# Kernel optimization log

Hardware: AMD Instinct MI355X
Metric: run time of the kernel (lower is better)

## Reference

```python
import jax, jax.numpy as jnp
import numpy as np

B, C, H, W = 4, 512, 64, 64
D = 512  # model_dim


def setup_inputs() -> dict:
    key = jax.random.key(0)
    ks = jax.random.split(key, 9)
    s = 0.02
    return {
        "q": jax.random.normal(ks[0], (B, C, H, W), dtype=jnp.float32),
        "Wq": jax.random.normal(ks[1], (D, C), dtype=jnp.float32) * s,
        "bq": jax.random.normal(ks[2], (D,), dtype=jnp.float32) * s,
        "Wk": jax.random.normal(ks[3], (D, C), dtype=jnp.float32) * s,
        "bk": jax.random.normal(ks[4], (D,), dtype=jnp.float32) * s,
        "Wv": jax.random.normal(ks[5], (D, C), dtype=jnp.float32) * s,
        "bv": jax.random.normal(ks[6], (D,), dtype=jnp.float32) * s,
        "Wo": jax.random.normal(ks[7], (C, D), dtype=jnp.float32) * s,
        "bo": jax.random.normal(ks[8], (C,), dtype=jnp.float32) * s,
    }


def reference(q, Wq, bq, Wk, bk, Wv, bv, Wo, bo):
    b, c, h, w = q.shape
    # 1x1 conv == per-pixel linear over channels; tokens s = h*w
    x = q.reshape(b, c, h * w)                      # (b, c, s)
    Q = jnp.einsum('bcs,dc->bsd', x, Wq) + bq       # (b, s, D)
    K = jnp.einsum('bcs,dc->bsd', x, Wk) + bk
    V = jnp.einsum('bcs,dc->bsd', x, Wv) + bv
    # ScaleAttend: scale = q.shape[-1]^-0.5 = model_dim^-0.5 (heads not split)
    scale = jnp.asarray(Q.shape[-1], Q.dtype) ** -0.5
    sim = jnp.einsum('bsd,btd->bst', Q, K) * scale  # (b, s, s)
    attn = jax.nn.softmax(sim, axis=-1)
    o = jnp.einsum('bst,btd->bsd', attn, V)         # (b, s, D)
    # to_out 1x1 conv: D -> C
    y = jnp.einsum('bsd,cd->bsc', o, Wo) + bo       # (b, s, C)
    return y.transpose(0, 2, 1).reshape(b, c, h, w)
```

## Files before the change

kernel.cpp:

```cpp
#include <hip/hip_runtime.h>
#include <hip/hip_bf16.h>

typedef __hip_bfloat16 bf16;
typedef __attribute__((ext_vector_type(8))) short short8;
typedef __attribute__((ext_vector_type(4))) float floatx4;
typedef __attribute__((ext_vector_type(4))) short shortx4;

static constexpr int BATCH = 4;
static constexpr int CH    = 512;
static constexpr int SEQ   = 4096;
static constexpr int DM    = 512;

__device__ __forceinline__ void gload16(const void* g, void* l) {
  __builtin_amdgcn_global_load_lds(
      (const __attribute__((address_space(1))) unsigned int*)g,
      (__attribute__((address_space(3))) unsigned int*)l,
      16, 0, 0);
}

__global__ __launch_bounds__(256) void cvt_weights(
    const float* __restrict__ w0, const float* __restrict__ w1,
    const float* __restrict__ w2, const float* __restrict__ w3,
    bf16* __restrict__ out) {
  const float* src = (blockIdx.y == 0) ? w0 : (blockIdx.y == 1) ? w1
                   : (blockIdx.y == 2) ? w2 : w3;
  int idx = blockIdx.x * 256 + threadIdx.x;
  out[(long)blockIdx.y * (DM * CH) + idx] = __float2bfloat16(src[idx]);
}

__global__ __launch_bounds__(256) void transpose_cvt(
    const float* __restrict__ x, bf16* __restrict__ xT) {
  __shared__ float tile[64][65];
  const int s0 = blockIdx.x * 64, c0 = blockIdx.y * 64;
  const float* xb = x + (long)blockIdx.z * CH * SEQ;
  bf16* xTb = xT + (long)blockIdx.z * SEQ * CH;
  const int t = threadIdx.x;
  const int sl = t & 63, cq = t >> 6;
  #pragma unroll
  for (int i = 0; i < 16; ++i) {
    int cl = cq * 16 + i;
    tile[cl][sl] = xb[(long)(c0 + cl) * SEQ + s0 + sl];
  }
  __syncthreads();
  const int cl2 = t & 63, sq = t >> 6;
  #pragma unroll
  for (int i = 0; i < 16; ++i) {
    int sl2 = sq * 16 + i;
    xTb[(long)(s0 + sl2) * CH + c0 + cl2] = __float2bfloat16(tile[cl2][sl2]);
  }
}

__global__ __launch_bounds__(512, 2) void gemm_qk(
    const bf16* __restrict__ A, long sAz,
    const bf16* __restrict__ B, long sBz,
    bf16* __restrict__ C, long sCz,
    float scale, int K, int ldc) {
  __shared__ __align__(16) bf16 As[2][256 * 64];
  __shared__ __align__(16) bf16 Bs[2][256 * 64];

  int id = blockIdx.x + gridDim.x * (blockIdx.y + gridDim.y * blockIdx.z);
  int nwg = gridDim.x * gridDim.y * gridDim.z;
  int sid = ((nwg & 7) == 0) ? ((id & 7) * (nwg >> 3) + (id >> 3)) : id;
  const int bx = sid % gridDim.x;
  const int by = (sid / gridDim.x) % gridDim.y;
  const int bz = sid / (gridDim.x * gridDim.y);

  const int tid = threadIdx.x;
  const long lK = K;
  const bf16* Ab = A + (long)bz * sAz + (long)by * 256 * lK;
  const bf16* Bb = B + (long)bz * sBz + (long)bx * 256 * lK;

  const int w = tid >> 6, lane = tid & 63;
  const int wr = w >> 2, wc = w & 3;
  const int l16 = lane & 15, quad = lane >> 4;

  const int srow = tid >> 3;
  const int sp = tid & 7;
  const int slog = (sp ^ (srow & 7)) << 3;

  const int pA0 = (quad ^ (l16 & 7)) << 3;
  const int pA1 = pA0 ^ 32;

  auto stageAh = [&](int buf, int kt, int h) {
    #pragma unroll
    for (int r = 0; r < 2; ++r) {
      const int row = h * 64 + r * 128 + srow;
      gload16(Ab + (long)kt * 64 + (long)row * lK + slog,
              (char*)(&As[buf][0]) + row * 128 + sp * 16);
    }
  };
  auto stageBh = [&](int buf, int kt, int h) {
    #pragma unroll
    for (int r = 0; r < 2; ++r) {
      const int row = h * 64 + r * 128 + srow;
      gload16(Bb + (long)kt * 64 + (long)row * lK + slog,
              (char*)(&Bs[buf][0]) + row * 128 + sp * 16);
    }
  };

  floatx4 acc[8][4];
  #pragma unroll
  for (int m = 0; m < 8; ++m)
    #pragma unroll
    for (int n = 0; n < 4; ++n) acc[m][n] = (floatx4)(0.0f);

  const int nk = K >> 6;
  stageBh(0, 0, 0); stageBh(0, 0, 1);
  stageAh(0, 0, 0); stageAh(0, 0, 1);
  asm volatile("s_waitcnt vmcnt(2)" ::: "memory");
  __builtin_amdgcn_s_barrier();

  for (int t = 0; t < nk; ++t) {
    const int cur = t & 1, nxt = cur ^ 1;
    const bf16* __restrict__ Al = &As[cur][0];
    const bf16* __restrict__ Bl = &Bs[cur][0];
    const bool more = (t + 1 < nk);
    short8 a[4], b[2][4];
    #pragma unroll
    for (int p = 0; p < 4; ++p) {
      const int qm = p >> 1, kc = p & 1;
      const int poff = kc ? pA1 : pA0;
      #pragma unroll
      for (int i = 0; i < 4; ++i) {
        const int ar = wr * 128 + qm * 64 + i * 16 + l16;
        a[i] = *(const short8*)(Al + ar * 64 + poff);
      }
      if (qm == 0) {
        #pragma unroll
        for (int j = 0; j < 4; ++j) {
          const int br = wc * 64 + j * 16 + l16;
          b[kc][j] = *(const short8*)(Bl + br * 64 + poff);
        }
      }
      if (more) {
        if (p == 0)      stageBh(nxt, t + 1, 0);
        else if (p == 1) stageBh(nxt, t + 1, 1);
        else if (p == 2) stageAh(nxt, t + 1, 0);
        else             stageAh(nxt, t + 1, 1);
      }
      __builtin_amdgcn_s_barrier();
      __builtin_amdgcn_s_setprio(1);
      #pragma unroll
      for (int i = 0; i < 4; ++i)
        #pragma unroll
        for (int j = 0; j < 4; ++j)
          acc[qm * 4 + i][j] = __builtin_amdgcn_mfma_f32_16x16x32_bf16(
              a[i], b[kc][j], acc[qm * 4 + i][j], 0, 0, 0);
      __builtin_amdgcn_s_setprio(0);
      if (p == 1) {
        if (more) asm volatile("s_waitcnt vmcnt(4)" ::: "memory");
        else      asm volatile("s_waitcnt vmcnt(0)" ::: "memory");
      } else if (p == 3 && more) {
        asm volatile("s_waitcnt vmcnt(2)" ::: "memory");
      }
      __builtin_amdgcn_s_barrier();
    }
  }

  bf16* Cb = C + (long)bz * sCz;
  const int rbase = by * 256 + wr * 128 + quad * 4;
  const int cbase = bx * 256 + wc * 64 + l16;
  #pragma unroll
  for (int m = 0; m < 8; ++m) {
    const int row = rbase + m * 16;
    #pragma unroll
    for (int n = 0; n < 4; ++n) {
      const int col = cbase + n * 16;
      floatx4 v = acc[m][n];
      #pragma unroll
      for (int r = 0; r < 4; ++r)
        Cb[(long)(row + r) * ldc + col] = __float2bfloat16(v[r] * scale);
    }
  }
}

template <int MODE>
__global__ __launch_bounds__(512, 2) void gemm_bn128(
    const bf16* __restrict__ A, long sAz,
    const bf16* __restrict__ B, long sBz,
    void* __restrict__ Cv, long sCz,
    const float* __restrict__ bias, float scale,
    int K, int ldc) {
  __shared__ __align__(16) bf16 As[3][256 * 64];
  __shared__ __align__(16) bf16 Bs[3][128 * 64];

  int id = blockIdx.x + gridDim.x * (blockIdx.y + gridDim.y * blockIdx.z);
  int nwg = gridDim.x * gridDim.y * gridDim.z;
  int sid = ((nwg & 7) == 0) ? ((id & 7) * (nwg >> 3) + (id >> 3)) : id;
  const int bx = sid % gridDim.x;
  const int by = (sid / gridDim.x) % gridDim.y;
  const int bz = sid / (gridDim.x * gridDim.y);

  const int tid = threadIdx.x;
  const long lK = K;
  const bf16* Ab = A + (long)bz * sAz + (long)by * 256 * lK;
  const bf16* Bb = B + (long)bz * sBz + (long)bx * 128 * lK;

  const int w = tid >> 6, lane = tid & 63;
  const int wr = w >> 1, wc = w & 1;
  const int l16 = lane & 15, quad = lane >> 4;

  const int srow = tid >> 3;
  const int sp = tid & 7;
  const int slog = (sp ^ (srow & 7)) << 3;

  const int pA0 = (quad ^ (l16 & 7)) << 3;
  const int pA1 = pA0 ^ 32;

  auto stageA = [&](int buf, int kt) {
    const bf16* s = Ab + (long)kt * 64 + (long)srow * lK + slog;
    char* d = (char*)(&As[buf][0]) + tid * 16;
    #pragma unroll
    for (int r = 0; r < 4; ++r)
      gload16(s + (long)(r * 64) * lK, d + r * 8192);
  };
  auto stageB = [&](int buf, int kt) {
    const bf16* s = Bb + (long)kt * 64 + (long)srow * lK + slog;
    char* d = (char*)(&Bs[buf][0]) + tid * 16;
    #pragma unroll
    for (int r = 0; r < 2; ++r)
      gload16(s + (long)(r * 64) * lK, d + r * 8192);
  };

  floatx4 acc[4][4];
  #pragma unroll
  for (int m = 0; m < 4; ++m)
    #pragma unroll
    for (int n = 0; n < 4; ++n) acc[m][n] = (floatx4)(0.0f);

  const int nk = K >> 6;
  stageA(0, 0); stageB(0, 0);
  stageA(1, 1); stageB(1, 1);
  asm volatile("s_waitcnt vmcnt(6)" ::: "memory");
  __builtin_amdgcn_s_barrier();

  int bcur = 0, bstage = 2;
  for (int t = 0; t < nk; ++t) {
    const bf16* __restrict__ Al = &As[bcur][0];
    const bf16* __restrict__ Bl = &Bs[bcur][0];
    const bool more = (t + 2 < nk);
    #pragma unroll
    for (int kc = 0; kc < 2; ++kc) {
      const int poff = kc ? pA1 : pA0;
      short8 a[4], b[4];
      #pragma unroll
      for (int i = 0; i < 4; ++i)
        a[i] = *(const short8*)(Al + (wr * 64 + i * 16 + l16) * 64 + poff);
      #pragma unroll
      for (int j = 0; j < 4; ++j)
        b[j] = *(const short8*)(Bl + (wc * 64 + j * 16 + l16) * 64 + poff);
      if (more) {
        if (kc == 0) stageA(bstage, t + 2);
        else         stageB(bstage, t + 2);
      }
      __builtin_amdgcn_s_barrier();
      __builtin_amdgcn_s_setprio(1);
      #pragma unroll
      for (int i = 0; i < 4; ++i)
        #pragma unroll
        for (int j = 0; j < 4; ++j)
          acc[i][j] = __builtin_amdgcn_mfma_f32_16x16x32_bf16(
              a[i], b[j], acc[i][j], 0, 0, 0);
      __builtin_amdgcn_s_setprio(0);
      if (kc == 1) {
        if (more)            asm volatile("s_waitcnt vmcnt(6)" ::: "memory");
        else if (t + 1 < nk) asm volatile("s_waitcnt vmcnt(0)" ::: "memory");
      }
      __builtin_amdgcn_s_barrier();
    }
    bcur = (bcur == 2) ? 0 : bcur + 1;
    bstage = (bstage == 2) ? 0 : bstage + 1;
  }

  const int rbase = by * 256 + wr * 64 + quad * 4;
  const int cbase = bx * 128 + wc * 64 + l16;
  #pragma unroll
  for (int m = 0; m < 4; ++m) {
    const int row = rbase + m * 16;
    #pragma unroll
    for (int n = 0; n < 4; ++n) {
      const int col = cbase + n * 16;
      floatx4 v = acc[m][n];
      if constexpr (MODE == 0) {
        bf16* C = (bf16*)Cv + (long)bz * sCz;
        const float bb = bias[col];
        #pragma unroll
        for (int r = 0; r < 4; ++r)
          C[(long)(row + r) * ldc + col] = __float2bfloat16(v[r] + bb);
      } else if constexpr (MODE == 1) {
        bf16* C = (bf16*)Cv + (long)bz * sCz;
        const float bb = bias[col];
        alignas(8) bf16 tmp[4];
        #pragma unroll
        for (int r = 0; r < 4; ++r) tmp[r] = __float2bfloat16(v[r] + bb);
        *(shortx4*)(C + (long)col * ldc + row) = *(const shortx4*)tmp;
      } else if constexpr (MODE == 2) {
        bf16* C = (bf16*)Cv + (long)bz * sCz;
        #pragma unroll
        for (int r = 0; r < 4; ++r)
          C[(long)(row + r) * ldc + col] = __float2bfloat16(v[r] * scale);
      } else {
        float* C = (float*)Cv + (long)bz * sCz;
        const float bb = bias[col];
        floatx4 o_;
        #pragma unroll
        for (int r = 0; r < 4; ++r) o_[r] = v[r] + bb;
        *(floatx4*)(C + (long)col * ldc + row) = o_;
      }
    }
  }
}

__global__ __launch_bounds__(256) void softmax_rows(bf16* __restrict__ sim) {
  bf16* p = sim + (long)blockIdx.y * ((long)SEQ * SEQ) + (long)blockIdx.x * SEQ;
  uint4* p4 = (uint4*)p;
  const int t = threadIdx.x;
  union U { uint4 u; ushort h[8]; } d[2];
  d[0].u = p4[t];
  d[1].u = p4[t + 256];
  float v[16];
  float mx = -3.0e38f;
  #pragma unroll
  for (int i = 0; i < 16; ++i) {
    v[i] = __uint_as_float(((unsigned)d[i >> 3].h[i & 7]) << 16);
    mx = fmaxf(mx, v[i]);
  }
  #pragma unroll
  for (int o = 32; o > 0; o >>= 1) mx = fmaxf(mx, __shfl_xor(mx, o));
  __shared__ float redmax[4], redsum[4];
  if ((t & 63) == 0) redmax[t >> 6] = mx;
  __syncthreads();
  mx = fmaxf(fmaxf(redmax[0], redmax[1]), fmaxf(redmax[2], redmax[3]));
  float sum = 0.f;
  #pragma unroll
  for (int i = 0; i < 16; ++i) {
    v[i] = __expf(v[i] - mx);
    sum += v[i];
  }
  #pragma unroll
  for (int o = 32; o > 0; o >>= 1) sum += __shfl_xor(sum, o);
  if ((t & 63) == 0) redsum[t >> 6] = sum;
  __syncthreads();
  sum = redsum[0] + redsum[1] + redsum[2] + redsum[3];
  const float inv = 1.0f / sum;
  union Hb { __hip_bfloat16 h; ushort u; };
  #pragma unroll
  for (int i = 0; i < 16; ++i) {
    Hb hb;
    hb.h = __float2bfloat16(v[i] * inv);
    d[i >> 3].h[i & 7] = hb.u;
  }
  p4[t] = d[0].u;
  p4[t + 256] = d[1].u;
}

extern "C" void kernel_launch(void* const* d_in, const int* in_sizes, int n_in,
                              void* d_out, int out_size, void* d_ws,
                              size_t ws_size, hipStream_t stream) {
  const float* q  = (const float*)d_in[0];
  const float* Wq = (const float*)d_in[1];
  const float* bq = (const float*)d_in[2];
  const float* Wk = (const float*)d_in[3];
  const float* bk = (const float*)d_in[4];
  const float* Wv = (const float*)d_in[5];
  const float* bv = (const float*)d_in[6];
  const float* Wo = (const float*)d_in[7];
  const float* bo = (const float*)d_in[8];
  float* out = (float*)d_out;

  bf16* ws = (bf16*)d_ws;
  const long WSZ = (long)DM * CH;
  const long XSZ = (long)SEQ * CH;
  const long SSZ = (long)SEQ * SEQ;
  bf16* Wqb = ws;
  bf16* Wkb = Wqb + WSZ;
  bf16* Wvb = Wqb + 2 * WSZ;
  bf16* Wob = Wqb + 3 * WSZ;
  bf16* xT  = Wqb + 4 * WSZ;
  bf16* Qb  = xT + BATCH * XSZ;
  bf16* Kb  = Qb + BATCH * XSZ;
  bf16* Vt  = Kb + BATCH * XSZ;
  bf16* Ob  = Vt + BATCH * XSZ;
  bf16* Sim = Ob + BATCH * XSZ;

  cvt_weights<<<dim3(WSZ / 256, 4), 256, 0, stream>>>(Wq, Wk, Wv, Wo, ws);
  transpose_cvt<<<dim3(SEQ / 64, CH / 64, BATCH), 256, 0, stream>>>(q, xT);

  gemm_bn128<0><<<dim3(4, 16, BATCH), 512, 0, stream>>>(
      xT, XSZ, Wqb, 0, Qb, XSZ, bq, 1.f, CH, DM);
  gemm_bn128<0><<<dim3(4, 16, BATCH), 512, 0, stream>>>(
      xT, XSZ, Wkb, 0, Kb, XSZ, bk, 1.f, CH, DM);
  gemm_bn128<1><<<dim3(4, 16, BATCH), 512, 0, stream>>>(
      xT, XSZ, Wvb, 0, Vt, XSZ, bv, 1.f, CH, SEQ);
  gemm_qk<<<dim3(16, 16, BATCH), 512, 0, stream>>>(
      Qb, XSZ, Kb, XSZ, Sim, SSZ, 0.04419417382415922f, CH, SEQ);
  softmax_rows<<<dim3(SEQ, BATCH), 256, 0, stream>>>(Sim);
  gemm_bn128<2><<<dim3(4, 16, BATCH), 512, 0, stream>>>(
      Sim, SSZ, Vt, XSZ, Ob, XSZ, nullptr, 1.0f, SEQ, DM);
  gemm_bn128<4><<<dim3(4, 16, BATCH), 512, 0, stream>>>(
      Ob, XSZ, Wob, 0, out, XSZ, bo, 1.f, DM, SEQ);
}
```

Baseline: 359.5 us.

## Restructure 256x256 GEMM into 8-phase ping-pong with split warp quadrants

Rewrites the 256x256 bf16 GEMM main loop. It now processes two K-tiles per outer iteration in an unrolled ping-pong over eight phases, issuing half-tile prefetches for tiles one and two steps ahead. It also remaps each warp's output tile from a contiguous 128x64 block to two 64-row by two 32-column sub-blocks, which changes the LDS read pattern and the epilogue store order. Explicit sched_barriers and lgkmcnt waits are added around the block barriers. The goal is deeper overlap of global-to-LDS loads with MFMA work, at the cost of more barriers, more complex waitcnt bookkeeping, and some risk of correctness issues when nk is odd.

```diff
diff --git a/kernel.cpp b/kernel.cpp
--- a/kernel.cpp
+++ b/kernel.cpp
@@ -81,97 +81,110 @@
   const int pA0 = (quad ^ (l16 & 7)) << 3;
   const int pA1 = pA0 ^ 32;
 
-  auto stageAh = [&](int buf, int kt, int h) {
+  auto stage_half = [&](const bf16* Gb, bf16* Lb, int kt, int h) {
     #pragma unroll
     for (int r = 0; r < 2; ++r) {
-      const int row = h * 64 + r * 128 + srow;
-      gload16(Ab + (long)kt * 64 + (long)row * lK + slog,
-              (char*)(&As[buf][0]) + row * 128 + sp * 16);
+      const int row = h * 128 + r * 64 + srow;
+      gload16(Gb + (long)kt * 64 + (long)row * lK + slog,
+              (char*)Lb + row * 128 + sp * 16);
     }
   };
-  auto stageBh = [&](int buf, int kt, int h) {
-    #pragma unroll
-    for (int r = 0; r < 2; ++r) {
-      const int row = h * 64 + r * 128 + srow;
-      gload16(Bb + (long)kt * 64 + (long)row * lK + slog,
-              (char*)(&Bs[buf][0]) + row * 128 + sp * 16);
+
+  floatx4 acc[8][4];
+  #pragma unroll
+  for (int m = 0; m < 8; ++m)
+    #pragma unroll
+    for (int n = 0; n < 4; ++n) acc[m][n] = (floatx4)(0.0f);
+
+  const int nk = K >> 6;
+  stage_half(Ab, &As[0][0], 0, 0); stage_half(Bb, &Bs[0][0], 0, 0);
+  stage_half(Ab, &As[0][0], 0, 1); stage_half(Bb, &Bs[0][0], 0, 1);
+  if (nk > 1) { stage_half(Ab, &As[1][0], 1, 0); stage_half(Bb, &Bs[1][0], 1, 0); }
+  asm volatile("s_waitcnt vmcnt(4)" ::: "memory");
+  __builtin_amdgcn_s_barrier();
+
+  for (int tt = 0; tt < nk; tt += 2) {
+    #pragma unroll
+    for (int u = 0; u < 2; ++u) {
+      const bf16* __restrict__ Al = &As[u][0];
+      const bf16* __restrict__ Bl = &Bs[u][0];
+      short8 a[2][4], b[2][2][2];
+      #pragma unroll
+      for (int p = 0; p < 4; ++p) {
+        const int rm = p >> 1, cn = p & 1;
+        if (cn == 0) {
+          #pragma unroll
+          for (int kc = 0; kc < 2; ++kc)
+            #pragma unroll
+            for (int i = 0; i < 4; ++i)
+              a[kc][i] = *(const short8*)(
+                  Al + (rm * 128 + wr * 64 + i * 16 + l16) * 64
+                     + (kc ? pA1 : pA0));
+        }
+        if (rm == 0) {
+          #pragma unroll
+          for (int kc = 0; kc < 2; ++kc)
+            #pragma unroll
+            for (int j = 0; j < 2; ++j)
+              b[kc][cn][j] = *(const short8*)(
+                  Bl + (cn * 128 + wc * 32 + j * 16 + l16) * 64
+                     + (kc ? pA1 : pA0));
+        }
+        {
+          const int g = u * 4 + p;
+          const int stile = tt + 1 + ((g + 2) >> 2);
+          if (stile < nk) {
+            const int sh = (p < 2) ? 1 : 0;
+            if (p & 1) stage_half(Bb, &Bs[stile & 1][0], stile, sh);
+            else       stage_half(Ab, &As[stile & 1][0], stile, sh);
+          }
+        }
+        __builtin_amdgcn_sched_barrier(0);
+        __builtin_amdgcn_s_barrier();
+        asm volatile("s_waitcnt lgkmcnt(0)" ::: "memory");
+        __builtin_amdgcn_sched_barrier(0);
+        __builtin_amdgcn_s_setprio(1);
+        #pragma unroll
+        for (int kc = 0; kc < 2; ++kc)
+          #pragma unroll
+          for (int i = 0; i < 4; ++i)
+            #pragma unroll
+            for (int j = 0; j < 2; ++j)
+              acc[rm * 4 + i][cn * 2 + j] =
+                  __builtin_amdgcn_mfma_f32_16x16x32_bf16(
+                      a[kc][i], b[kc][cn][j], acc[rm * 4 + i][cn * 2 + j],
+                      0, 0, 0);
+        __builtin_amdgcn_s_setprio(0);
+        if (p == 3) {
+          if (u == 0) {
+            if (tt + 2 < nk) asm volatile("s_waitcnt vmcnt(4)" ::: "memory");
+            else             asm volatile("s_waitcnt vmcnt(0)" ::: "memory");
+          } else {
+            if (tt + 2 < nk) asm volatile("s_waitcnt vmcnt(4)" ::: "memory");
+          }
+        }
+        __builtin_amdgcn_s_barrier();
+      }
     }
-  };
-
-  floatx4 acc[8][4];
-  #pragma unroll
-  for (int m = 0; m < 8; ++m)
-    #pragma unroll
-    for (int n = 0; n < 4; ++n) acc[m][n] = (floatx4)(0.0f);
-
-  const int nk = K >> 6;
-  stageBh(0, 0, 0); stageBh(0, 0, 1);
-  stageAh(0, 0, 0); stageAh(0, 0, 1);
-  asm volatile("s_waitcnt vmcnt(2)" ::: "memory");
-  __builtin_amdgcn_s_barrier();
-
-  for (int t = 0; t < nk; ++t) {
-    const int cur = t & 1, nxt = cur ^ 1;
-    const bf16* __restrict__ Al = &As[cur][0];
-    const bf16* __restrict__ Bl = &Bs[cur][0];
-    const bool more = (t + 1 < nk);
-    short8 a[4], b[2][4];
-    #pragma unroll
-    for (int p = 0; p < 4; ++p) {
-      const int qm = p >> 1, kc = p & 1;
-      const int poff = kc ? pA1 : pA0;
+  }
+
+  bf16* Cb = C + (long)bz * sCz;
+  #pragma unroll
+  for (int rm = 0; rm < 2; ++rm)
+    #pragma unroll
+    for (int i = 0; i < 4; ++i) {
+      const int row = by * 256 + rm * 128 + wr * 64 + i * 16 + quad * 4;
       #pragma unroll
-      for (int i = 0; i < 4; ++i) {
-        const int ar = wr * 128 + qm * 64 + i * 16 + l16;
-        a[i] = *(const short8*)(Al + ar * 64 + poff);
-      }
-      if (qm == 0) {
-        #pragma unroll
-        for (int j = 0; j < 4; ++j) {
-          const int br = wc * 64 + j * 16 + l16;
-          b[kc][j] = *(const short8*)(Bl + br * 64 + poff);
+      for (int cn = 0; cn < 2; ++cn)
+        #pragma unroll
+        for (int j = 0; j < 2; ++j) {
+          const int col = bx * 256 + cn * 128 + wc * 32 + j * 16 + l16;
+          floatx4 v = acc[rm * 4 + i][cn * 2 + j];
+          #pragma unroll
+          for (int r = 0; r < 4; ++r)
+            Cb[(long)(row + r) * ldc + col] = __float2bfloat16(v[r] * scale);
         }
-      }
-      if (more) {
-        if (p == 0)      stageBh(nxt, t + 1, 0);
-        else if (p == 1) stageBh(nxt, t + 1, 1);
-        else if (p == 2) stageAh(nxt, t + 1, 0);
-        else             stageAh(nxt, t + 1, 1);
-      }
-      __builtin_amdgcn_s_barrier();
-      __builtin_amdgcn_s_setprio(1);
-      #pragma unroll
-      for (int i = 0; i < 4; ++i)
-        #pragma unroll
-        for (int j = 0; j < 4; ++j)
-          acc[qm * 4 + i][j] = __builtin_amdgcn_mfma_f32_16x16x32_bf16(
-              a[i], b[kc][j], acc[qm * 4 + i][j], 0, 0, 0);
-      __builtin_amdgcn_s_setprio(0);
-      if (p == 1) {
-        if (more) asm volatile("s_waitcnt vmcnt(4)" ::: "memory");
-        else      asm volatile("s_waitcnt vmcnt(0)" ::: "memory");
-      } else if (p == 3 && more) {
-        asm volatile("s_waitcnt vmcnt(2)" ::: "memory");
-      }
-      __builtin_amdgcn_s_barrier();
     }
-  }
-
-  bf16* Cb = C + (long)bz * sCz;
-  const int rbase = by * 256 + wr * 128 + quad * 4;
-  const int cbase = bx * 256 + wc * 64 + l16;
-  #pragma unroll
-  for (int m = 0; m < 8; ++m) {
-    const int row = rbase + m * 16;
-    #pragma unroll
-    for (int n = 0; n < 4; ++n) {
-      const int col = cbase + n * 16;
-      floatx4 v = acc[m][n];
-      #pragma unroll
-      for (int r = 0; r < 4; ++r)
-        Cb[(long)(row + r) * ldc + col] = __float2bfloat16(v[r] * scale);
-    }
-  }
 }
 
 template <int MODE>
```

Measured after the change: 362.8 us. Within noise of the previous version (+0.9%).
